# Kernel tuning notes

Measured on AMD Instinct MI355X. Metric: run time of the kernel, lower is better.

Reference implementation:

```python
import jax, jax.numpy as jnp
import numpy as np

INPUT_DIM = 16
NUM_MFS = 4
NUM_RULES = 1024
NUM_CLASSES = 10
BATCH = 4096


def setup_inputs() -> dict:
    key = jax.random.key(0)
    k1, k2, k3, k4, k5 = jax.random.split(key, 5)
    x = jax.random.normal(k1, (BATCH, INPUT_DIM), dtype=jnp.float32)
    centers = jax.random.normal(k2, (INPUT_DIM, NUM_MFS), dtype=jnp.float32)
    # widths must be positive (used as std of gaussian)
    widths = jax.random.uniform(k3, (INPUT_DIM, NUM_MFS), dtype=jnp.float32, minval=0.2, maxval=1.2)
    consequents = jax.random.normal(k4, (NUM_RULES, INPUT_DIM + 1, NUM_CLASSES), dtype=jnp.float32)
    rule_idx = jax.random.randint(k5, (INPUT_DIM, NUM_RULES), 0, NUM_MFS, dtype=jnp.int32)
    return {"x": x, "centers": centers, "widths": widths,
            "consequents": consequents, "rule_idx": rule_idx}


def reference(x, centers, widths, consequents, rule_idx):
    B, D = x.shape
    # Gaussian membership functions: [B, D, M]
    mfs = jnp.exp(-((x[:, :, None] - centers[None]) ** 2) / (2.0 * widths[None] ** 2) + 1e-9)
    # Gather rule-specific memberships: [B, D, R]
    d_idx = jnp.arange(D)[:, None]  # [D, 1] broadcasts with rule_idx [D, R]
    rule_mfs = mfs[:, d_idx, rule_idx]
    # Firing strengths (product over input dims) and normalization: [B, R]
    firing = jnp.prod(rule_mfs, axis=1)
    norm_fs = firing / (jnp.sum(firing, axis=1, keepdims=True) + 1e-9)
    # Extended input with bias column: [B, D+1]
    x_ext = jnp.concatenate([x, jnp.ones((B, 1), dtype=x.dtype)], axis=1)
    # phi = norm_fs[:, :, None] * x_ext[:, None, :]; y = phi_flat @ beta_flat
    # expressed as a single contraction (same math, phi is detached w.r.t. x_ext)
    y_hat = jnp.einsum('br,bi,ric->bc', norm_fs, jax.lax.stop_gradient(x_ext), consequents)
    return y_hat, norm_fs, x_ext
```

## Files before the change

### kernel.cpp

```cpp
#include <hip/hip_runtime.h>

#define B 4096
#define D 16
#define R 1024
#define NC 10
#define IC 170
#define NT 11
#define NP 176
#define KSPLIT 8
#define RPB (R / KSPLIT)
#define BT 64
#define BSTR 136
#define GSP 180

typedef __attribute__((ext_vector_type(8))) short short8;
typedef __attribute__((ext_vector_type(4))) float f32x4;

__device__ __forceinline__ unsigned short f2bf(float f) {
    unsigned u = __float_as_uint(f);
    return (unsigned short)((u + 0x7fffu + ((u >> 16) & 1u)) >> 16);
}

__global__ __launch_bounds__(256) void prep_kernel(
    const float* __restrict__ cons, unsigned short* __restrict__ Bsw,
    const int* __restrict__ rule_idx, unsigned* __restrict__ packed,
    float* __restrict__ out_y)
{
    const int bid = blockIdx.x, tid = threadIdx.x;
    if (bid < 704) {
        int t = bid * 256 + tid;
        int row = t >> 10;
        int k   = t & 1023;
        float v = (row < IC) ? cons[(size_t)k * IC + row] : 0.0f;
        Bsw[t] = f2bf(v);
    } else if (bid < 708) {
        int r = (bid - 704) * 256 + tid;
        unsigned bits = 0;
#pragma unroll
        for (int d = 0; d < D; ++d)
            bits |= (((unsigned)rule_idx[d * R + r]) & 3u) << (2 * d);
        packed[r] = bits;
    } else {
        out_y[(bid - 708) * 256 + tid] = 0.0f;
    }
}

__global__ __launch_bounds__(256) void firing_kernel(
    const float* __restrict__ x, const float* __restrict__ centers,
    const float* __restrict__ widths, const unsigned* __restrict__ packed,
    float* __restrict__ out_norm, float* __restrict__ out_xext)
{
    __shared__ float2 s_z2[8][16];
    __shared__ float2 s_z4[4 * 256];
    __shared__ float2 s_red[4];
    const int tid = threadIdx.x;
    const int b0 = blockIdx.x * 2, b1 = b0 + 1;
    const int lane = tid & 63, wv = tid >> 6;

    float z0, z1;
    {
        int d = lane >> 2;
        float c = centers[lane], w = widths[lane];
        float xv0 = x[(size_t)b0 * D + d];
        float xv1 = x[(size_t)b1 * D + d];
        float d0 = xv0 - c, d1 = xv1 - c;
        z0 = 1e-9f - d0 * d0 / (2.0f * w * w);
        z1 = 1e-9f - d1 * d1 / (2.0f * w * w);
    }
    if (tid < 34) {
        int si = tid / 17, i = tid - si * 17;
        int bb = b0 + si;
        out_xext[(size_t)bb * 17 + i] = (i < 16) ? x[(size_t)bb * D + i] : 1.0f;
    }
    if (wv < 2) {
        int p = tid >> 4, i = tid & 15;
        int la = p * 8 + (i & 3);
        int lb = p * 8 + 4 + ((i >> 2) & 3);
        float za0 = __shfl(z0, la, 64), zb0 = __shfl(z0, lb, 64);
        float za1 = __shfl(z1, la, 64), zb1 = __shfl(z1, lb, 64);
        float2 v; v.x = za0 + zb0; v.y = za1 + zb1;
        s_z2[p][i] = v;
    }
    __syncthreads();
#pragma unroll
    for (int q = 0; q < 4; ++q) {
        float2 a = s_z2[2 * q][tid & 15];
        float2 c = s_z2[2 * q + 1][(tid >> 4) & 15];
        float2 v; v.x = a.x + c.x; v.y = a.y + c.y;
        s_z4[q * 256 + tid] = v;
    }
    __syncthreads();

    uint4 pw = *(const uint4*)&packed[4 * tid];
    unsigned wq[4] = {pw.x, pw.y, pw.z, pw.w};
    float f0[4], f1[4], l0 = 0.0f, l1 = 0.0f;
#pragma unroll
    for (int k = 0; k < 4; ++k) {
        unsigned wk = wq[k];
        float2 g0 = s_z4[wk & 255];
        float2 g1 = s_z4[256 + ((wk >> 8) & 255)];
        float2 g2 = s_z4[512 + ((wk >> 16) & 255)];
        float2 g3 = s_z4[768 + (wk >> 24)];
        float s0 = g0.x + g1.x + g2.x + g3.x;
        float s1 = g0.y + g1.y + g2.y + g3.y;
        f0[k] = __expf(s0);
        f1[k] = __expf(s1);
        l0 += f0[k];
        l1 += f1[k];
    }
#pragma unroll
    for (int off = 1; off < 64; off <<= 1) {
        l0 += __shfl_xor(l0, off, 64);
        l1 += __shfl_xor(l1, off, 64);
    }
    if (lane == 0) { float2 v; v.x = l0; v.y = l1; s_red[wv] = v; }
    __syncthreads();
    const float inv0 = 1.0f / (s_red[0].x + s_red[1].x + s_red[2].x + s_red[3].x + 1e-9f);
    const float inv1 = 1.0f / (s_red[0].y + s_red[1].y + s_red[2].y + s_red[3].y + 1e-9f);
    float4 o0, o1;
    o0.x = f0[0] * inv0; o0.y = f0[1] * inv0; o0.z = f0[2] * inv0; o0.w = f0[3] * inv0;
    o1.x = f1[0] * inv1; o1.y = f1[1] * inv1; o1.z = f1[2] * inv1; o1.w = f1[3] * inv1;
    *(float4*)&out_norm[(size_t)b0 * R + 4 * tid] = o0;
    *(float4*)&out_norm[(size_t)b1 * R + 4 * tid] = o1;
}

__global__ __launch_bounds__(256, 2) void yhat_kernel(
    const float* __restrict__ norm, const unsigned short* __restrict__ Bsw,
    const float* __restrict__ x, float* __restrict__ out_y)
{
    __shared__ unsigned short Bs[NP * BSTR];
    __shared__ unsigned short As[BT * BSTR];
    __shared__ float xe[BT * 17];

    const int tid = threadIdx.x;
    const int mt = blockIdx.x & 63;
    const int ks = blockIdx.x >> 6;
    const int bl0 = mt * BT;
    const int kabs = ks * RPB;

    for (int t = tid; t < BT * 17; t += 256) {
        int bl = t / 17, i = t - bl * 17;
        xe[t] = (i < 16) ? x[(size_t)(bl0 + bl) * D + i] : 1.0f;
    }
    for (int t = tid; t < NP * 16; t += 256) {
        int row = t >> 4, seg = t & 15;
        *(short8*)&Bs[row * BSTR + seg * 8] =
            *(const short8*)&Bsw[row * R + kabs + seg * 8];
    }
    for (int t = tid; t < BT * 32; t += 256) {
        int row = t >> 5, c4 = t & 31;
        float4 v = *(const float4*)&norm[(size_t)(bl0 + row) * R + kabs + c4 * 4];
        ushort4 o;
        o.x = f2bf(v.x); o.y = f2bf(v.y); o.z = f2bf(v.z); o.w = f2bf(v.w);
        *(ushort4*)&As[row * BSTR + c4 * 4] = o;
    }
    __syncthreads();

    const int lane = tid & 63, wv = tid >> 6;
    const int m_ = lane & 15, q_ = lane >> 4;
    const int nt0 = wv * 3;
    const int ntn = (wv == 3) ? 2 : 3;

    f32x4 acc[4][3];
    const f32x4 zf = {0.f, 0.f, 0.f, 0.f};
#pragma unroll
    for (int mb = 0; mb < 4; ++mb)
#pragma unroll
        for (int j = 0; j < 3; ++j) acc[mb][j] = zf;

#pragma unroll
    for (int kh = 0; kh < 4; ++kh) {
        short8 a[4];
#pragma unroll
        for (int mb = 0; mb < 4; ++mb)
            a[mb] = *(const short8*)&As[(mb * 16 + m_) * BSTR + kh * 32 + q_ * 8];
#pragma unroll
        for (int j = 0; j < 3; ++j) {
            if (j < ntn) {
                short8 bfrag = *(const short8*)&Bs[((nt0 + j) * 16 + m_) * BSTR + kh * 32 + q_ * 8];
#pragma unroll
                for (int mb = 0; mb < 4; ++mb)
                    acc[mb][j] = __builtin_amdgcn_mfma_f32_16x16x32_bf16(a[mb], bfrag, acc[mb][j], 0, 0, 0);
            }
        }
    }

    __syncthreads();
    float* Gs = (float*)Bs;
#pragma unroll
    for (int j = 0; j < 3; ++j) {
        if (j < ntn) {
            int nt = nt0 + j;
#pragma unroll
            for (int mb = 0; mb < 4; ++mb)
#pragma unroll
                for (int r = 0; r < 4; ++r)
                    Gs[(mb * 16 + q_ * 4 + r) * GSP + nt * 16 + m_] = acc[mb][j][r];
        }
    }
    __syncthreads();
    for (int t = tid; t < BT * NC; t += 256) {
        int bl = t / NC, c = t - bl * NC;
        float y = 0.0f;
#pragma unroll
        for (int i = 0; i < 17; ++i)
            y += xe[bl * 17 + i] * Gs[bl * GSP + i * NC + c];
        atomicAdd(&out_y[(size_t)(bl0 + bl) * NC + c], y);
    }
}

extern "C" void kernel_launch(void* const* d_in, const int* in_sizes, int n_in,
                              void* d_out, int out_size, void* d_ws, size_t ws_size,
                              hipStream_t stream) {
    const float* x        = (const float*)d_in[0];
    const float* centers  = (const float*)d_in[1];
    const float* widths   = (const float*)d_in[2];
    const float* cons     = (const float*)d_in[3];
    const int*   rule_idx = (const int*)d_in[4];

    float* out      = (float*)d_out;
    float* out_y    = out;
    float* out_norm = out + (size_t)B * NC;
    float* out_xext = out + (size_t)B * NC + (size_t)B * R;

    unsigned* packed     = (unsigned*)d_ws;
    unsigned short* Bsw  = (unsigned short*)((char*)d_ws + 4096);

    prep_kernel<<<868, 256, 0, stream>>>(cons, Bsw, rule_idx, packed, out_y);
    firing_kernel<<<B / 2, 256, 0, stream>>>(x, centers, widths, packed,
                                             out_norm, out_xext);
    yhat_kernel<<<(B / BT) * KSPLIT, 256, 0, stream>>>(out_norm, Bsw, x, out_y);
}
```

Baseline: 90.34 us.

## Emit bf16 copy of normalized firing strengths and feed GEMM from global directly

The firing kernel now also writes a bf16 copy of the normalized firing strengths to workspace. A new yhat kernel reads its A fragments straight from that bf16 buffer in global memory instead of re-reading fp32 norms, converting them and staging them in LDS. The aim is to halve the GEMM's A-operand traffic and free LDS so three blocks can fit per CU. The cost is an extra 8 MB write in the firing kernel and uncoalesced-ish direct global fragment loads, and the fallback depends on workspace size.

```diff
diff --git a/kernel.cpp b/kernel.cpp
--- a/kernel.cpp
+++ b/kernel.cpp
@@ -48,7 +48,8 @@
 __global__ __launch_bounds__(256) void firing_kernel(
     const float* __restrict__ x, const float* __restrict__ centers,
     const float* __restrict__ widths, const unsigned* __restrict__ packed,
-    float* __restrict__ out_norm, float* __restrict__ out_xext)
+    float* __restrict__ out_norm, float* __restrict__ out_xext,
+    unsigned short* __restrict__ norm_b16)
 {
     __shared__ float2 s_z2[8][16];
     __shared__ float2 s_z4[4 * 256];
@@ -122,6 +123,91 @@
     o1.x = f1[0] * inv1; o1.y = f1[1] * inv1; o1.z = f1[2] * inv1; o1.w = f1[3] * inv1;
     *(float4*)&out_norm[(size_t)b0 * R + 4 * tid] = o0;
     *(float4*)&out_norm[(size_t)b1 * R + 4 * tid] = o1;
+    if (norm_b16) {
+        ushort4 h0, h1;
+        h0.x = f2bf(o0.x); h0.y = f2bf(o0.y); h0.z = f2bf(o0.z); h0.w = f2bf(o0.w);
+        h1.x = f2bf(o1.x); h1.y = f2bf(o1.y); h1.z = f2bf(o1.z); h1.w = f2bf(o1.w);
+        *(ushort4*)&norm_b16[(size_t)b0 * R + 4 * tid] = h0;
+        *(ushort4*)&norm_b16[(size_t)b1 * R + 4 * tid] = h1;
+    }
+}
+
+__global__ __launch_bounds__(256, 3) void yhat_kernel2(
+    const unsigned short* __restrict__ normb, const unsigned short* __restrict__ Bsw,
+    const float* __restrict__ x, float* __restrict__ out_y)
+{
+    __shared__ unsigned short Bs[NP * BSTR];
+    __shared__ float xe[BT * 17];
+
+    const int tid = threadIdx.x;
+    const int mt = blockIdx.x & 63;
+    const int ks = blockIdx.x >> 6;
+    const int bl0 = mt * BT;
+    const int kabs = ks * RPB;
+
+    for (int t = tid; t < BT * 17; t += 256) {
+        int bl = t / 17, i = t - bl * 17;
+        xe[t] = (i < 16) ? x[(size_t)(bl0 + bl) * D + i] : 1.0f;
+    }
+    for (int t = tid; t < NP * 16; t += 256) {
+        int row = t >> 4, seg = t & 15;
+        *(short8*)&Bs[row * BSTR + seg * 8] =
+            *(const short8*)&Bsw[row * R + kabs + seg * 8];
+    }
+    __syncthreads();
+
+    const int lane = tid & 63, wv = tid >> 6;
+    const int m_ = lane & 15, q_ = lane >> 4;
+    const int nt0 = wv * 3;
+    const int ntn = (wv == 3) ? 2 : 3;
+
+    f32x4 acc[4][3];
+    const f32x4 zf = {0.f, 0.f, 0.f, 0.f};
+#pragma unroll
+    for (int mb = 0; mb < 4; ++mb)
+#pragma unroll
+        for (int j = 0; j < 3; ++j) acc[mb][j] = zf;
+
+#pragma unroll
+    for (int kh = 0; kh < 4; ++kh) {
+        short8 a[4];
+#pragma unroll
+        for (int mb = 0; mb < 4; ++mb)
+            a[mb] = *(const short8*)&normb[(size_t)(bl0 + mb * 16 + m_) * R
+                                           + kabs + kh * 32 + q_ * 8];
+#pragma unroll
+        for (int j = 0; j < 3; ++j) {
+            if (j < ntn) {
+                short8 bfrag = *(const short8*)&Bs[((nt0 + j) * 16 + m_) * BSTR + kh * 32 + q_ * 8];
+#pragma unroll
+                for (int mb = 0; mb < 4; ++mb)
+                    acc[mb][j] = __builtin_amdgcn_mfma_f32_16x16x32_bf16(a[mb], bfrag, acc[mb][j], 0, 0, 0);
+            }
+        }
+    }
+
+    __syncthreads();
+    float* Gs = (float*)Bs;
+#pragma unroll
+    for (int j = 0; j < 3; ++j) {
+        if (j < ntn) {
+            int nt = nt0 + j;
+#pragma unroll
+            for (int mb = 0; mb < 4; ++mb)
+#pragma unroll
+                for (int r = 0; r < 4; ++r)
+                    Gs[(mb * 16 + q_ * 4 + r) * GSP + nt * 16 + m_] = acc[mb][j][r];
+        }
+    }
+    __syncthreads();
+    for (int t = tid; t < BT * NC; t += 256) {
+        int bl = t / NC, c = t - bl * NC;
+        float y = 0.0f;
+#pragma unroll
+        for (int i = 0; i < 17; ++i)
+            y += xe[bl * 17 + i] * Gs[bl * GSP + i * NC + c];
+        atomicAdd(&out_y[(size_t)(bl0 + bl) * NC + c], y);
+    }
 }
 
 __global__ __launch_bounds__(256, 2) void yhat_kernel(
@@ -225,9 +311,16 @@
 
     unsigned* packed     = (unsigned*)d_ws;
     unsigned short* Bsw  = (unsigned short*)((char*)d_ws + 4096);
+    const size_t NB16_OFF = 4096 + 360448;
+    const size_t need = NB16_OFF + (size_t)B * R * 2;
+    unsigned short* normb = (ws_size >= need)
+        ? (unsigned short*)((char*)d_ws + NB16_OFF) : nullptr;
 
     prep_kernel<<<868, 256, 0, stream>>>(cons, Bsw, rule_idx, packed, out_y);
     firing_kernel<<<B / 2, 256, 0, stream>>>(x, centers, widths, packed,
-                                             out_norm, out_xext);
-    yhat_kernel<<<(B / BT) * KSPLIT, 256, 0, stream>>>(out_norm, Bsw, x, out_y);
-}
+                                             out_norm, out_xext, normb);
+    if (normb)
+        yhat_kernel2<<<(B / BT) * KSPLIT, 256, 0, stream>>>(normb, Bsw, x, out_y);
+    else
+        yhat_kernel<<<(B / BT) * KSPLIT, 256, 0, stream>>>(out_norm, Bsw, x, out_y);
+}
```

Measured after the change: 87.26 us. 3.4% less time.
